# Kernel optimization log

Measured on AMD Instinct MI355X. Metric: run time of the kernel, lower is better.

Reference implementation:

```python
import jax, jax.numpy as jnp
import numpy as np

N, DEG, F_IN, F_OUT, H = 8192, 16, 1024, 128, 8


def setup_inputs() -> dict:
    key = jax.random.key(0)
    ks = jax.random.split(key, 6)
    features = jax.random.normal(ks[0], (N, F_IN), dtype=jnp.float32)
    adj = jax.random.randint(ks[1], (N, DEG), 0, N)  # fixed-degree adjacency
    W = jax.random.normal(ks[2], (H, F_IN, F_OUT), dtype=jnp.float32) / np.sqrt(F_IN)
    bW = jax.random.normal(ks[3], (H, F_OUT), dtype=jnp.float32) * 0.01
    a = jax.random.normal(ks[4], (H, 2 * F_OUT), dtype=jnp.float32) / np.sqrt(2.0 * F_OUT)
    ba = jax.random.normal(ks[5], (H,), dtype=jnp.float32) * 0.01
    return {"features": features, "adj": adj, "W": W, "bW": bW, "a": a, "ba": ba}


def reference(features, adj, W, bW, a, ba):
    n = features.shape[0]
    # neighbors with self appended last (matches adjlist[node] + [node])
    nbr = jnp.concatenate([adj, jnp.arange(n)[:, None]], axis=1)  # [N, DEG+1]
    # per-head linear transform: h[k] = features @ W_k + b_k
    h = jnp.einsum('nf,hfo->hno', features, W) + bW[:, None, :]  # [H, N, F_OUT]
    # attention score a_k([h_dst, h_src]) + bias decomposed into dst/src parts
    a_dst, a_src = a[:, :F_OUT], a[:, F_OUT:]
    s_dst = jnp.einsum('hno,ho->hn', h, a_dst)  # [H, N]
    s_src = jnp.einsum('hno,ho->hn', h, a_src)  # [H, N]
    scores = s_dst[:, :, None] + s_src[:, nbr] + ba[:, None, None]  # [H, N, DEG+1]
    scores = jax.nn.leaky_relu(scores, 0.2)
    alpha = jax.nn.softmax(scores, axis=-1)  # softmax over neighbors (incl. self)
    h_src = h[:, nbr]  # [H, N, DEG+1, F_OUT]
    out = jnp.einsum('hnd,hndf->hnf', alpha, h_src)  # [H, N, F_OUT]
    # concat heads along feature dim -> [N, H*F_OUT]
    return out.transpose(1, 0, 2).reshape(n, H * F_OUT)
```

## Files before the change

### kernel.cpp

```cpp
#include <hip/hip_runtime.h>
#include <hip/hip_bf16.h>

#define N_NODES 8192
#define DEG     16
#define F_IN    1024
#define F_OUT   128
#define NH      8

typedef __bf16 bf16x8 __attribute__((ext_vector_type(8)));
typedef float  f32x4  __attribute__((ext_vector_type(4)));

__device__ __forceinline__ float bf2f(unsigned short u) {
    union { unsigned int i; float f; } v;
    v.i = ((unsigned int)u) << 16;
    return v.f;
}
__device__ __forceinline__ unsigned short f2bf(float f) {
    union { float f; unsigned int u; } v; v.f = f;
    unsigned int u = v.u + 0x7FFFu + ((v.u >> 16) & 1u);
    return (unsigned short)(u >> 16);
}
__device__ __forceinline__ int detect_bf16(const unsigned int* __restrict__ w) {
    int hits = 0;
#pragma unroll
    for (int i = 0; i < 64; ++i) {
        unsigned int x = w[i * 131 + 17];
        int e = (x >> 7) & 0xFF;
        hits += (e >= 100 && e <= 140) ? 1 : 0;
    }
    return hits > 32;
}
__device__ __forceinline__ float rd_scalar(const void* p, int idx, int isbf) {
    return isbf ? bf2f(((const unsigned short*)p)[idx]) : ((const float*)p)[idx];
}
__device__ __forceinline__ void gload16(const void* g, void* l) {
    __builtin_amdgcn_global_load_lds(
        (const __attribute__((address_space(1))) void*)g,
        (__attribute__((address_space(3))) void*)l, 16, 0, 0);
}

__global__ __launch_bounds__(256) void prep_inputs(
    const void* __restrict__ feat, const void* __restrict__ W,
    unsigned short* __restrict__ featb, unsigned short* __restrict__ Wt)
{
    const int isbf = detect_bf16((const unsigned int*)feat);
    if (blockIdx.x < 4096) {
        size_t i8 = ((size_t)blockIdx.x * 256 + threadIdx.x) * 8;
        if (isbf) {
            *(uint4*)(featb + i8) = ((const uint4*)feat)[i8 / 8];
        } else {
            const float* s = (const float*)feat + i8;
            float4 u0 = *(const float4*)s;
            float4 u1 = *(const float4*)(s + 4);
            unsigned short t[8] = { f2bf(u0.x), f2bf(u0.y), f2bf(u0.z), f2bf(u0.w),
                                    f2bf(u1.x), f2bf(u1.y), f2bf(u1.z), f2bf(u1.w) };
            *(uint4*)(featb + i8) = *(const uint4*)t;
        }
    } else {
        __shared__ float tile[64][65];
        const int bx = blockIdx.x - 4096;
        const int h  = bx >> 5;
        const int kt = (bx >> 1) & 15;
        const int ot = bx & 1;
        const int t  = threadIdx.x;
#pragma unroll
        for (int i = 0; i < 16; ++i) {
            int id = i * 256 + t, r = id >> 6, c = id & 63;
            tile[r][c] = rd_scalar(W, ((h * 1024 + kt * 64 + r) * 128) + ot * 64 + c, isbf);
        }
        __syncthreads();
#pragma unroll
        for (int i = 0; i < 16; ++i) {
            int id = i * 256 + t, oc = id >> 6, kc = id & 63;
            Wt[(size_t)(h * 128 + ot * 64 + oc) * 1024 + kt * 64 + kc] = f2bf(tile[kc][oc]);
        }
    }
}

__global__ __launch_bounds__(256) void gat_gemm3(
    const unsigned short* __restrict__ featb,
    const unsigned short* __restrict__ Wt,
    const void* __restrict__ raw_feat,
    const void* __restrict__ bW, const void* __restrict__ a,
    const void* __restrict__ ba,
    __hip_bfloat16* __restrict__ hbuf,
    float* __restrict__ sdst, float* __restrict__ ssrc)
{
    const int rawbf = detect_bf16((const unsigned int*)raw_feat);

    const int h   = blockIdx.y;
    const int n0  = blockIdx.x * 128;
    const int tid = threadIdx.x;

    __shared__ __align__(16) unsigned short As[2][128 * 64];
    __shared__ __align__(16) unsigned short Bs[2][128 * 64];

    const int lane = tid & 63;
    const int wave = tid >> 6;
    const int quad = lane >> 4;
    const int l16  = lane & 15;
    const int sw   = l16 & 7;

    f32x4 acc[2][8];
#pragma unroll
    for (int i = 0; i < 2; ++i)
#pragma unroll
        for (int j = 0; j < 8; ++j) acc[i][j] = (f32x4)0.f;

    const unsigned short* wbase = Wt + (size_t)h * F_OUT * F_IN;

    for (int k0 = 0; k0 < F_IN; k0 += 128) {
#pragma unroll
        for (int p = 0; p < 2; ++p) {
            const int kk0 = k0 + p * 64;
#pragma unroll
            for (int t = 0; t < 4; ++t) {
                const int r0  = t * 32 + wave * 8;
                const int row = r0 + (lane >> 3);
                const int gc  = (lane & 7) ^ (row & 7);
                gload16(&featb[(size_t)(n0 + row) * F_IN + kk0 + gc * 8],
                        &As[p][r0 * 64]);
                gload16(&wbase[(size_t)row * F_IN + kk0 + gc * 8],
                        &Bs[p][r0 * 64]);
            }
        }
        __syncthreads();

#pragma unroll
        for (int p = 0; p < 2; ++p) {
#pragma unroll
            for (int ks = 0; ks < 2; ++ks) {
                const int kc = ks * 4 + quad;
                const int cs = (kc ^ sw) * 8;
                bf16x8 af[2], bfr[8];
#pragma unroll
                for (int rt = 0; rt < 2; ++rt)
                    af[rt] = *(const bf16x8*)&As[p][(wave * 32 + rt * 16 + l16) * 64 + cs];
#pragma unroll
                for (int ct = 0; ct < 8; ++ct)
                    bfr[ct] = *(const bf16x8*)&Bs[p][(ct * 16 + l16) * 64 + cs];
#pragma unroll
                for (int rt = 0; rt < 2; ++rt)
#pragma unroll
                    for (int ct = 0; ct < 8; ++ct)
                        acc[rt][ct] = __builtin_amdgcn_mfma_f32_16x16x32_bf16(
                            af[rt], bfr[ct], acc[rt][ct], 0, 0, 0);
            }
        }
        __syncthreads();
    }

#pragma unroll
    for (int ct = 0; ct < 8; ++ct) {
        const int col = ct * 16 + l16;
        const float bwv = rd_scalar(bW, h * F_OUT + col, rawbf);
#pragma unroll
        for (int rt = 0; rt < 2; ++rt) {
            const int nrow = n0 + wave * 32 + rt * 16 + quad * 4;
            __hip_bfloat16* dst = hbuf + ((size_t)h * N_NODES + nrow) * F_OUT + col;
#pragma unroll
            for (int r = 0; r < 4; ++r)
                dst[(size_t)r * F_OUT] = __float2bfloat16(acc[rt][ct][r] + bwv);
        }
    }

    float adst[8], asrc[8];
#pragma unroll
    for (int ct = 0; ct < 8; ++ct) {
        const int col = ct * 16 + l16;
        adst[ct] = rd_scalar(a, h * 256 + col, rawbf);
        asrc[ct] = rd_scalar(a, h * 256 + 128 + col, rawbf);
    }
    float pd[2][4] = {}, ps[2][4] = {};
#pragma unroll
    for (int rt = 0; rt < 2; ++rt)
#pragma unroll
        for (int ct = 0; ct < 8; ++ct)
#pragma unroll
            for (int r = 0; r < 4; ++r) {
                pd[rt][r] += acc[rt][ct][r] * adst[ct];
                ps[rt][r] += acc[rt][ct][r] * asrc[ct];
            }
#pragma unroll
    for (int off = 1; off < 16; off <<= 1)
#pragma unroll
        for (int rt = 0; rt < 2; ++rt)
#pragma unroll
            for (int r = 0; r < 4; ++r) {
                pd[rt][r] += __shfl_xor(pd[rt][r], off, 64);
                ps[rt][r] += __shfl_xor(ps[rt][r], off, 64);
            }
    if (l16 == 0) {
        const float bav = rd_scalar(ba, h, rawbf);
#pragma unroll
        for (int rt = 0; rt < 2; ++rt) {
            const int base = n0 + wave * 32 + rt * 16 + quad * 4;
            float4 vd = { pd[rt][0] + bav, pd[rt][1] + bav,
                          pd[rt][2] + bav, pd[rt][3] + bav };
            float4 vs = { ps[rt][0], ps[rt][1], ps[rt][2], ps[rt][3] };
            *(float4*)&sdst[h * N_NODES + base] = vd;
            *(float4*)&ssrc[h * N_NODES + base] = vs;
        }
    }
}

__global__ __launch_bounds__(256) void gat_aggr4(
    const unsigned short* __restrict__ hbuf,
    const int* __restrict__ adj,
    const float* __restrict__ sdst, const float* __restrict__ ssrc,
    const void* __restrict__ raw_feat, void* __restrict__ out)
{
    const int isbf = detect_bf16((const unsigned int*)raw_feat);
    const int h    = blockIdx.x;
    const int wave = threadIdx.x >> 6;
    const int lane = threadIdx.x & 63;
    const int half = lane >> 5;
    const int l32  = lane & 31;
    const int n    = blockIdx.y * 8 + wave * 2 + half;

    int nbr = n;
    if (l32 < DEG) nbr = adj[n * DEG + l32];

    float s = -1e30f;
    if (l32 < 17) {
        float sv = sdst[h * N_NODES + n] + ssrc[h * N_NODES + nbr];
        s = sv > 0.f ? sv : 0.2f * sv;
    }
    float m = s;
#pragma unroll
    for (int off = 1; off < 32; off <<= 1)
        m = fmaxf(m, __shfl_xor(m, off, 64));
    float ev = (l32 < 17) ? __expf(s - m) : 0.f;
    float sum = ev;
#pragma unroll
    for (int off = 1; off < 32; off <<= 1)
        sum += __shfl_xor(sum, off, 64);
    ev *= (1.f / sum);

    const unsigned short* hb = hbuf + (size_t)h * N_NODES * F_OUT;
    const int fc    = l32 * 4;
    const int sbase = half << 5;
    float a0 = 0.f, a1 = 0.f, a2 = 0.f, a3 = 0.f;
#pragma unroll
    for (int d = 0; d < 17; ++d) {
        const int   nb = __shfl(nbr, sbase + d, 64);
        const float av = __shfl(ev,  sbase + d, 64);
        uint2 pk = *(const uint2*)&hb[(size_t)nb * F_OUT + fc];
        a0 += av * bf2f((unsigned short)(pk.x & 0xffffu));
        a1 += av * bf2f((unsigned short)(pk.x >> 16));
        a2 += av * bf2f((unsigned short)(pk.y & 0xffffu));
        a3 += av * bf2f((unsigned short)(pk.y >> 16));
    }

    const size_t oidx = (size_t)n * (NH * F_OUT) + h * F_OUT + fc;
    if (isbf) {
        uint2 res;
        res.x = (unsigned int)f2bf(a0) | ((unsigned int)f2bf(a1) << 16);
        res.y = (unsigned int)f2bf(a2) | ((unsigned int)f2bf(a3) << 16);
        *(uint2*)&((unsigned short*)out)[oidx] = res;
    } else {
        float4 res = { a0, a1, a2, a3 };
        *(float4*)&((float*)out)[oidx] = res;
    }
}

__global__ __launch_bounds__(256) void gat_gemm_fb(
    const void* __restrict__ feat, const void* __restrict__ W,
    const void* __restrict__ bW, __hip_bfloat16* __restrict__ hbuf)
{
    const int isbf = detect_bf16((const unsigned int*)feat);
    const int h = blockIdx.y, n0 = blockIdx.x * 128, tid = threadIdx.x;
    __shared__ __align__(16) unsigned short As[128][72];
    __shared__ __align__(16) unsigned short Bs[128][72];
    const int lane = tid & 63, wave = tid >> 6, quad = lane >> 4, l16 = lane & 15;
    f32x4 acc[2][8];
#pragma unroll
    for (int i = 0; i < 2; ++i)
#pragma unroll
        for (int j = 0; j < 8; ++j) acc[i][j] = (f32x4)0.f;
    for (int k0 = 0; k0 < F_IN; k0 += 64) {
        if (isbf) {
            const unsigned short* fbase = (const unsigned short*)feat + (size_t)n0 * F_IN;
            const unsigned short* wsrc  = (const unsigned short*)W +
                                          (size_t)h * F_IN * F_OUT + (size_t)k0 * F_OUT;
#pragma unroll
            for (int t = 0; t < 4; ++t) {
                int c = t * 256 + tid, row = c >> 3, kc = c & 7;
                *(uint4*)&As[row][kc * 8] = *(const uint4*)&fbase[row * F_IN + k0 + kc * 8];
            }
#pragma unroll
            for (int t = 0; t < 2; ++t) {
                int c = t * 256 + tid, kr2 = c >> 4, mm = c & 15, oc = mm * 8;
                uint4 w0 = *(const uint4*)&wsrc[(2 * kr2) * F_OUT + oc];
                uint4 w1 = *(const uint4*)&wsrc[(2 * kr2 + 1) * F_OUT + oc];
                const unsigned short* p0 = (const unsigned short*)&w0;
                const unsigned short* p1 = (const unsigned short*)&w1;
#pragma unroll
                for (int j = 0; j < 8; ++j) {
                    int i = (j + mm) & 7;
                    *(unsigned int*)&Bs[oc + i][2 * kr2] =
                        (unsigned int)p0[i] | ((unsigned int)p1[i] << 16);
                }
            }
        } else {
            const float* fbase = (const float*)feat + (size_t)n0 * F_IN;
            const float* wsrc  = (const float*)W +
                                 (size_t)h * F_IN * F_OUT + (size_t)k0 * F_OUT;
#pragma unroll
            for (int t = 0; t < 4; ++t) {
                int c = t * 256 + tid, row = c >> 3, kc = c & 7;
                const float* src = &fbase[row * F_IN + k0 + kc * 8];
                float4 u0 = *(const float4*)src, u1 = *(const float4*)(src + 4);
                unsigned short sh[8] = { f2bf(u0.x), f2bf(u0.y), f2bf(u0.z), f2bf(u0.w),
                                         f2bf(u1.x), f2bf(u1.y), f2bf(u1.z), f2bf(u1.w) };
                *(uint4*)&As[row][kc * 8] = *(const uint4*)sh;
            }
#pragma unroll
            for (int t = 0; t < 2; ++t) {
                int c = t * 256 + tid, kr2 = c >> 4, mm = c & 15, oc = mm * 8;
                const float* r0 = &wsrc[(2 * kr2) * F_OUT + oc];
                const float* r1 = &wsrc[(2 * kr2 + 1) * F_OUT + oc];
                float4 e0 = *(const float4*)r0, e1 = *(const float4*)(r0 + 4);
                float4 o0 = *(const float4*)r1, o1 = *(const float4*)(r1 + 4);
                unsigned short p0[8] = { f2bf(e0.x), f2bf(e0.y), f2bf(e0.z), f2bf(e0.w),
                                         f2bf(e1.x), f2bf(e1.y), f2bf(e1.z), f2bf(e1.w) };
                unsigned short p1[8] = { f2bf(o0.x), f2bf(o0.y), f2bf(o0.z), f2bf(o0.w),
                                         f2bf(o1.x), f2bf(o1.y), f2bf(o1.z), f2bf(o1.w) };
#pragma unroll
                for (int j = 0; j < 8; ++j) {
                    int i = (j + mm) & 7;
                    *(unsigned int*)&Bs[oc + i][2 * kr2] =
                        (unsigned int)p0[i] | ((unsigned int)p1[i] << 16);
                }
            }
        }
        __syncthreads();
#pragma unroll
        for (int ks = 0; ks < 2; ++ks) {
            const int kk = ks * 32 + quad * 8;
            bf16x8 af[2], bfr[8];
#pragma unroll
            for (int rt = 0; rt < 2; ++rt)
                af[rt] = *(const bf16x8*)&As[wave * 32 + rt * 16 + l16][kk];
#pragma unroll
            for (int ct = 0; ct < 8; ++ct)
                bfr[ct] = *(const bf16x8*)&Bs[ct * 16 + l16][kk];
#pragma unroll
            for (int rt = 0; rt < 2; ++rt)
#pragma unroll
                for (int ct = 0; ct < 8; ++ct)
                    acc[rt][ct] = __builtin_amdgcn_mfma_f32_16x16x32_bf16(
                        af[rt], bfr[ct], acc[rt][ct], 0, 0, 0);
        }
        __syncthreads();
    }
#pragma unroll
    for (int ct = 0; ct < 8; ++ct) {
        const int col = ct * 16 + l16;
        const float bwv = rd_scalar(bW, h * F_OUT + col, isbf);
#pragma unroll
        for (int rt = 0; rt < 2; ++rt) {
            const int nrow = n0 + wave * 32 + rt * 16 + quad * 4;
            __hip_bfloat16* dst = hbuf + ((size_t)h * N_NODES + nrow) * F_OUT + col;
#pragma unroll
            for (int r = 0; r < 4; ++r)
                dst[(size_t)r * F_OUT] = __float2bfloat16(acc[rt][ct][r] + bwv);
        }
    }
}

__global__ __launch_bounds__(256) void gat_aggr_fb(
    const __hip_bfloat16* __restrict__ hbuf, const int* __restrict__ adj,
    const void* __restrict__ a, const void* __restrict__ ba,
    void* __restrict__ out, const void* __restrict__ feat)
{
    const int isbf = detect_bf16((const unsigned int*)feat);
    const int n = blockIdx.x, wave = threadIdx.x >> 6, lane = threadIdx.x & 63;
    const int hh = blockIdx.y * 4 + wave;
    int nbr_reg = n;
    if (lane < DEG) nbr_reg = adj[n * DEG + lane];
    const int f0 = lane * 2;
    const float adst0 = rd_scalar(a, hh * 256 + f0, isbf);
    const float adst1 = rd_scalar(a, hh * 256 + f0 + 1, isbf);
    const float asrc0 = rd_scalar(a, hh * 256 + 128 + f0, isbf);
    const float asrc1 = rd_scalar(a, hh * 256 + 128 + f0 + 1, isbf);
    const float bav   = rd_scalar(ba, hh, isbf);
    const __hip_bfloat16* hb = hbuf + (size_t)hh * N_NODES * F_OUT;
    float v0[17], v1[17], red[18];
#pragma unroll
    for (int d = 0; d < 17; ++d) {
        int nb = __shfl(nbr_reg, d, 64);
        unsigned int pk = *(const unsigned int*)&hb[(size_t)nb * F_OUT + f0];
        v0[d] = bf2f((unsigned short)(pk & 0xffffu));
        v1[d] = bf2f((unsigned short)(pk >> 16));
        red[d] = v0[d] * asrc0 + v1[d] * asrc1;
    }
    red[17] = v0[16] * adst0 + v1[16] * adst1;
#pragma unroll
    for (int off = 1; off < 64; off <<= 1)
#pragma unroll
        for (int r = 0; r < 18; ++r) red[r] += __shfl_xor(red[r], off, 64);
    const float sd = red[17] + bav;
    float sc[17], mx = -1e30f;
#pragma unroll
    for (int d = 0; d < 17; ++d) {
        float s = sd + red[d];
        s = s > 0.f ? s : 0.2f * s;
        sc[d] = s; mx = fmaxf(mx, s);
    }
    float ssum = 0.f;
#pragma unroll
    for (int d = 0; d < 17; ++d) { sc[d] = __expf(sc[d] - mx); ssum += sc[d]; }
    const float inv = 1.f / ssum;
    float o0 = 0.f, o1 = 0.f;
#pragma unroll
    for (int d = 0; d < 17; ++d) { o0 += sc[d] * v0[d]; o1 += sc[d] * v1[d]; }
    o0 *= inv; o1 *= inv;
    const size_t oidx = (size_t)n * (NH * F_OUT) + hh * F_OUT + f0;
    if (isbf) {
        *(unsigned int*)&((unsigned short*)out)[oidx] =
            (unsigned int)f2bf(o0) | ((unsigned int)f2bf(o1) << 16);
    } else {
        float2 res; res.x = o0; res.y = o1;
        *(float2*)&((float*)out)[oidx] = res;
    }
}

extern "C" void kernel_launch(void* const* d_in, const int* in_sizes, int n_in,
                              void* d_out, int out_size, void* d_ws, size_t ws_size,
                              hipStream_t stream)
{
    const void* feat = d_in[0];
    const int*  adj  = (const int*)d_in[1];
    const void* W    = d_in[2];
    const void* bW   = d_in[3];
    const void* a    = d_in[4];
    const void* ba   = d_in[5];

    char* ws = (char*)d_ws;
    __hip_bfloat16* hbuf = (__hip_bfloat16*)ws;
    const size_t HB = (size_t)NH * N_NODES * F_OUT * 2;
    const size_t SC = (size_t)NH * N_NODES * 4;
    float* sdst = (float*)(ws + HB);
    float* ssrc = (float*)(ws + HB + SC);
    unsigned short* featb = (unsigned short*)(ws + HB + 2 * SC);
    unsigned short* Wt    = featb + (size_t)N_NODES * F_IN;
    const size_t needA = HB + 2 * SC +
        ((size_t)N_NODES * F_IN + (size_t)NH * F_IN * F_OUT) * 2;

    if (ws_size >= needA) {
        prep_inputs<<<4352, 256, 0, stream>>>(feat, W, featb, Wt);
        gat_gemm3<<<dim3(64, 8), 256, 0, stream>>>(featb, Wt, feat, bW, a, ba,
                                                   hbuf, sdst, ssrc);
        gat_aggr4<<<dim3(8, 1024), 256, 0, stream>>>((const unsigned short*)hbuf,
                                                     adj, sdst, ssrc, feat, d_out);
    } else {
        gat_gemm_fb<<<dim3(64, 8), 256, 0, stream>>>(feat, W, bW, hbuf);
        gat_aggr_fb<<<dim3(8192, 2), 256, 0, stream>>>(hbuf, adj, a, ba, d_out, feat);
    }
}
```

Before: 149.0 us.

## Rewrite GEMM with 256x128 tiles, 8 waves, and 3-stage async load pipeline

Replaces the 128x128, 4-wave GEMM with a 256x128 tile per block using 8 waves arranged as a 4x2 grid, and a triple-buffered shared-memory pipeline. Global loads for later K-tiles are issued while MFMAs run on the current tile, coordinated by explicit vmcnt waits and raw barriers. s_setprio is raised around the MFMA bursts. The attention-score dot products now need a cross-wave reduction through shared memory. The aim is to hide global load latency and improve reuse. In exchange, shared memory use grows to about 144KB. The grid also halves to 256 blocks, which may underfill the GPU's compute units.

```diff
diff --git a/kernel.cpp b/kernel.cpp
--- a/kernel.cpp
+++ b/kernel.cpp
@@ -77,7 +77,7 @@
     }
 }
 
-__global__ __launch_bounds__(256) void gat_gemm3(
+__global__ __launch_bounds__(512, 2) void gat_gemm4(
     const unsigned short* __restrict__ featb,
     const unsigned short* __restrict__ Wt,
     const void* __restrict__ raw_feat,
@@ -89,118 +89,138 @@
     const int rawbf = detect_bf16((const unsigned int*)raw_feat);
 
     const int h   = blockIdx.y;
-    const int n0  = blockIdx.x * 128;
+    const int n0  = blockIdx.x * 256;
     const int tid = threadIdx.x;
 
-    __shared__ __align__(16) unsigned short As[2][128 * 64];
-    __shared__ __align__(16) unsigned short Bs[2][128 * 64];
+    __shared__ __align__(16) unsigned short As[3][256 * 64];
+    __shared__ __align__(16) unsigned short Bs[3][128 * 64];
+    __shared__ float sred[4][2][2][64];
 
     const int lane = tid & 63;
     const int wave = tid >> 6;
+    const int wr   = wave >> 1;
+    const int wc   = wave & 1;
     const int quad = lane >> 4;
     const int l16  = lane & 15;
-    const int sw   = l16 & 7;
-
-    f32x4 acc[2][8];
-#pragma unroll
-    for (int i = 0; i < 2; ++i)
-#pragma unroll
-        for (int j = 0; j < 8; ++j) acc[i][j] = (f32x4)0.f;
+    const int srow   = lane >> 3;
+    const int schunk = lane & 7;
+
+    f32x4 acc[4][4];
+#pragma unroll
+    for (int i = 0; i < 4; ++i)
+#pragma unroll
+        for (int j = 0; j < 4; ++j) acc[i][j] = (f32x4)0.f;
 
     const unsigned short* wbase = Wt + (size_t)h * F_OUT * F_IN;
 
-    for (int k0 = 0; k0 < F_IN; k0 += 128) {
-#pragma unroll
-        for (int p = 0; p < 2; ++p) {
-            const int kk0 = k0 + p * 64;
-#pragma unroll
-            for (int t = 0; t < 4; ++t) {
-                const int r0  = t * 32 + wave * 8;
-                const int row = r0 + (lane >> 3);
-                const int gc  = (lane & 7) ^ (row & 7);
-                gload16(&featb[(size_t)(n0 + row) * F_IN + kk0 + gc * 8],
-                        &As[p][r0 * 64]);
-                gload16(&wbase[(size_t)row * F_IN + kk0 + gc * 8],
-                        &Bs[p][r0 * 64]);
-            }
-        }
-        __syncthreads();
-
-#pragma unroll
-        for (int p = 0; p < 2; ++p) {
-#pragma unroll
-            for (int ks = 0; ks < 2; ++ks) {
-                const int kc = ks * 4 + quad;
-                const int cs = (kc ^ sw) * 8;
-                bf16x8 af[2], bfr[8];
-#pragma unroll
-                for (int rt = 0; rt < 2; ++rt)
-                    af[rt] = *(const bf16x8*)&As[p][(wave * 32 + rt * 16 + l16) * 64 + cs];
-#pragma unroll
-                for (int ct = 0; ct < 8; ++ct)
-                    bfr[ct] = *(const bf16x8*)&Bs[p][(ct * 16 + l16) * 64 + cs];
-#pragma unroll
-                for (int rt = 0; rt < 2; ++rt)
-#pragma unroll
-                    for (int ct = 0; ct < 8; ++ct)
-                        acc[rt][ct] = __builtin_amdgcn_mfma_f32_16x16x32_bf16(
-                            af[rt], bfr[ct], acc[rt][ct], 0, 0, 0);
-            }
-        }
-        __syncthreads();
-    }
-
-#pragma unroll
-    for (int ct = 0; ct < 8; ++ct) {
-        const int col = ct * 16 + l16;
-        const float bwv = rd_scalar(bW, h * F_OUT + col, rawbf);
-#pragma unroll
-        for (int rt = 0; rt < 2; ++rt) {
-            const int nrow = n0 + wave * 32 + rt * 16 + quad * 4;
-            __hip_bfloat16* dst = hbuf + ((size_t)h * N_NODES + nrow) * F_OUT + col;
-#pragma unroll
-            for (int r = 0; r < 4; ++r)
-                dst[(size_t)r * F_OUT] = __float2bfloat16(acc[rt][ct][r] + bwv);
-        }
-    }
-
-    float adst[8], asrc[8];
-#pragma unroll
-    for (int ct = 0; ct < 8; ++ct) {
-        const int col = ct * 16 + l16;
+    auto stage = [&](int kt, int s) {
+        if (kt >= 16) return;
+        const int kk0 = kt * 64;
+#pragma unroll
+        for (int t = 0; t < 4; ++t) {
+            const int r0  = t * 64 + wave * 8;
+            const int row = r0 + srow;
+            const int gc  = schunk ^ (row & 7);
+            gload16(&featb[(size_t)(n0 + row) * F_IN + kk0 + gc * 8],
+                    &As[s][r0 * 64]);
+        }
+#pragma unroll
+        for (int t = 0; t < 2; ++t) {
+            const int r0  = t * 64 + wave * 8;
+            const int row = r0 + srow;
+            const int gc  = schunk ^ (row & 7);
+            gload16(&wbase[(size_t)row * F_IN + kk0 + gc * 8],
+                    &Bs[s][r0 * 64]);
+        }
+    };
+
+    stage(0, 0);
+    stage(1, 1);
+
+    for (int t = 0; t < 16; ++t) {
+        stage(t + 2, (t + 2) % 3);
+        if (t < 14)       asm volatile("s_waitcnt vmcnt(12)" ::: "memory");
+        else if (t == 14) asm volatile("s_waitcnt vmcnt(6)"  ::: "memory");
+        else              asm volatile("s_waitcnt vmcnt(0)"  ::: "memory");
+        asm volatile("s_barrier" ::: "memory");
+
+        const unsigned short* Ab = As[t % 3];
+        const unsigned short* Bb = Bs[t % 3];
+#pragma unroll
+        for (int ks = 0; ks < 2; ++ks) {
+            const int kc = ks * 4 + quad;
+            const int cs = (kc ^ (l16 & 7)) * 8;
+            bf16x8 af[4], bfr[4];
+#pragma unroll
+            for (int rt = 0; rt < 4; ++rt)
+                af[rt] = *(const bf16x8*)&Ab[(wr * 64 + rt * 16 + l16) * 64 + cs];
+#pragma unroll
+            for (int ct = 0; ct < 4; ++ct)
+                bfr[ct] = *(const bf16x8*)&Bb[(wc * 64 + ct * 16 + l16) * 64 + cs];
+            __builtin_amdgcn_s_setprio(1);
+#pragma unroll
+            for (int rt = 0; rt < 4; ++rt)
+#pragma unroll
+                for (int ct = 0; ct < 4; ++ct)
+                    acc[rt][ct] = __builtin_amdgcn_mfma_f32_16x16x32_bf16(
+                        af[rt], bfr[ct], acc[rt][ct], 0, 0, 0);
+            __builtin_amdgcn_s_setprio(0);
+        }
+        asm volatile("s_barrier" ::: "memory");
+    }
+
+    float adst[4], asrc[4];
+#pragma unroll
+    for (int ct = 0; ct < 4; ++ct) {
+        const int col = wc * 64 + ct * 16 + l16;
         adst[ct] = rd_scalar(a, h * 256 + col, rawbf);
         asrc[ct] = rd_scalar(a, h * 256 + 128 + col, rawbf);
     }
-    float pd[2][4] = {}, ps[2][4] = {};
-#pragma unroll
-    for (int rt = 0; rt < 2; ++rt)
-#pragma unroll
-        for (int ct = 0; ct < 8; ++ct)
+    float pd[4][4] = {}, ps[4][4] = {};
+#pragma unroll
+    for (int ct = 0; ct < 4; ++ct) {
+        const int col = wc * 64 + ct * 16 + l16;
+        const float bwv = rd_scalar(bW, h * F_OUT + col, rawbf);
+#pragma unroll
+        for (int rt = 0; rt < 4; ++rt) {
+            const int nrow = n0 + wr * 64 + rt * 16 + quad * 4;
+            __hip_bfloat16* dst = hbuf + ((size_t)h * N_NODES + nrow) * F_OUT + col;
 #pragma unroll
             for (int r = 0; r < 4; ++r) {
+                dst[(size_t)r * F_OUT] = __float2bfloat16(acc[rt][ct][r] + bwv);
                 pd[rt][r] += acc[rt][ct][r] * adst[ct];
                 ps[rt][r] += acc[rt][ct][r] * asrc[ct];
             }
+        }
+    }
 #pragma unroll
     for (int off = 1; off < 16; off <<= 1)
 #pragma unroll
-        for (int rt = 0; rt < 2; ++rt)
+        for (int rt = 0; rt < 4; ++rt)
 #pragma unroll
             for (int r = 0; r < 4; ++r) {
                 pd[rt][r] += __shfl_xor(pd[rt][r], off, 64);
                 ps[rt][r] += __shfl_xor(ps[rt][r], off, 64);
             }
     if (l16 == 0) {
+#pragma unroll
+        for (int rt = 0; rt < 4; ++rt)
+#pragma unroll
+            for (int r = 0; r < 4; ++r) {
+                const int row64 = rt * 16 + quad * 4 + r;
+                sred[wr][wc][0][row64] = pd[rt][r];
+                sred[wr][wc][1][row64] = ps[rt][r];
+            }
+    }
+    __syncthreads();
+    if (wc == 0) {
         const float bav = rd_scalar(ba, h, rawbf);
-#pragma unroll
-        for (int rt = 0; rt < 2; ++rt) {
-            const int base = n0 + wave * 32 + rt * 16 + quad * 4;
-            float4 vd = { pd[rt][0] + bav, pd[rt][1] + bav,
-                          pd[rt][2] + bav, pd[rt][3] + bav };
-            float4 vs = { ps[rt][0], ps[rt][1], ps[rt][2], ps[rt][3] };
-            *(float4*)&sdst[h * N_NODES + base] = vd;
-            *(float4*)&ssrc[h * N_NODES + base] = vs;
-        }
+        const int row64 = lane;
+        const float vd = sred[wr][0][0][row64] + sred[wr][1][0][row64] + bav;
+        const float vs = sred[wr][0][1][row64] + sred[wr][1][1][row64];
+        const int nrow = n0 + wr * 64 + row64;
+        sdst[h * N_NODES + nrow] = vd;
+        ssrc[h * N_NODES + nrow] = vs;
     }
 }
 
@@ -450,7 +470,7 @@
 
     if (ws_size >= needA) {
         prep_inputs<<<4352, 256, 0, stream>>>(feat, W, featb, Wt);
-        gat_gemm3<<<dim3(64, 8), 256, 0, stream>>>(featb, Wt, feat, bW, a, ba,
+        gat_gemm4<<<dim3(32, 8), 512, 0, stream>>>(featb, Wt, feat, bW, a, ba,
                                                    hbuf, sdst, ssrc);
         gat_aggr4<<<dim3(8, 1024), 256, 0, stream>>>((const unsigned short*)hbuf,
                                                      adj, sdst, ssrc, feat, d_out);
```

Result: slower. 157.0 us (+5.4%).

## Double-buffer GEMM K-tiles to overlap global loads with MFMA compute

Applied to the files above, without the earlier changes.

The projection GEMM's main loop used to load two 64-wide K slices, synchronize, compute both, then synchronize again, so loads and math never overlapped. It now runs a software pipeline over 16 K-tiles of 64. The next tile is loaded into the alternate LDS buffer while the current tile is computed, with one barrier per iteration. This is meant to hide global-to-LDS latency behind MFMA work. In exchange there are twice as many loop iterations and barriers, each with less work, and correctness depends on the async loads landing before the barrier.

```diff
diff --git a/kernel.cpp b/kernel.cpp
--- a/kernel.cpp
+++ b/kernel.cpp
@@ -100,6 +100,8 @@
     const int quad = lane >> 4;
     const int l16  = lane & 15;
     const int sw   = l16 & 7;
+    const int srow   = lane >> 3;
+    const int schunk = lane & 7;
 
     f32x4 acc[2][8];
 #pragma unroll
@@ -109,45 +111,48 @@
 
     const unsigned short* wbase = Wt + (size_t)h * F_OUT * F_IN;
 
-    for (int k0 = 0; k0 < F_IN; k0 += 128) {
-#pragma unroll
-        for (int p = 0; p < 2; ++p) {
-            const int kk0 = k0 + p * 64;
-#pragma unroll
-            for (int t = 0; t < 4; ++t) {
-                const int r0  = t * 32 + wave * 8;
-                const int row = r0 + (lane >> 3);
-                const int gc  = (lane & 7) ^ (row & 7);
-                gload16(&featb[(size_t)(n0 + row) * F_IN + kk0 + gc * 8],
-                        &As[p][r0 * 64]);
-                gload16(&wbase[(size_t)row * F_IN + kk0 + gc * 8],
-                        &Bs[p][r0 * 64]);
-            }
-        }
+    auto stage = [&](int kt, int s) {
+        const int kk0 = kt * 64;
+#pragma unroll
+        for (int t = 0; t < 4; ++t) {
+            const int r0  = t * 32 + wave * 8;
+            const int row = r0 + srow;
+            const int gc  = schunk ^ (row & 7);
+            gload16(&featb[(size_t)(n0 + row) * F_IN + kk0 + gc * 8],
+                    &As[s][r0 * 64]);
+            gload16(&wbase[(size_t)row * F_IN + kk0 + gc * 8],
+                    &Bs[s][r0 * 64]);
+        }
+    };
+
+    stage(0, 0);
+    __syncthreads();
+
+    int cur = 0;
+    for (int t = 0; t < 16; ++t) {
+        if (t < 15) stage(t + 1, cur ^ 1);
+
+#pragma unroll
+        for (int ks = 0; ks < 2; ++ks) {
+            const int kc = ks * 4 + quad;
+            const int cs = (kc ^ sw) * 8;
+            bf16x8 af[2], bfr[8];
+#pragma unroll
+            for (int rt = 0; rt < 2; ++rt)
+                af[rt] = *(const bf16x8*)&As[cur][(wave * 32 + rt * 16 + l16) * 64 + cs];
+#pragma unroll
+            for (int ct = 0; ct < 8; ++ct)
+                bfr[ct] = *(const bf16x8*)&Bs[cur][(ct * 16 + l16) * 64 + cs];
+#pragma unroll
+            for (int rt = 0; rt < 2; ++rt)
+#pragma unroll
+                for (int ct = 0; ct < 8; ++ct)
+                    acc[rt][ct] = __builtin_amdgcn_mfma_f32_16x16x32_bf16(
+                        af[rt], bfr[ct], acc[rt][ct], 0, 0, 0);
+        }
+
         __syncthreads();
-
-#pragma unroll
-        for (int p = 0; p < 2; ++p) {
-#pragma unroll
-            for (int ks = 0; ks < 2; ++ks) {
-                const int kc = ks * 4 + quad;
-                const int cs = (kc ^ sw) * 8;
-                bf16x8 af[2], bfr[8];
-#pragma unroll
-                for (int rt = 0; rt < 2; ++rt)
-                    af[rt] = *(const bf16x8*)&As[p][(wave * 32 + rt * 16 + l16) * 64 + cs];
-#pragma unroll
-                for (int ct = 0; ct < 8; ++ct)
-                    bfr[ct] = *(const bf16x8*)&Bs[p][(ct * 16 + l16) * 64 + cs];
-#pragma unroll
-                for (int rt = 0; rt < 2; ++rt)
-#pragma unroll
-                    for (int ct = 0; ct < 8; ++ct)
-                        acc[rt][ct] = __builtin_amdgcn_mfma_f32_16x16x32_bf16(
-                            af[rt], bfr[ct], acc[rt][ct], 0, 0, 0);
-            }
-        }
-        __syncthreads();
+        cur ^= 1;
     }
 
 #pragma unroll
```

After: 154.6 us. +3.8%, slower.

## Fuse prep, GEMM and aggregation into one persistent kernel with grid barriers

Applied to the files above, without the earlier changes.

Three kernel launches are replaced by a single persistent kernel of 512 blocks. The blocks step through the input conversion, the per-head GEMM and the neighbor aggregation, with atomic-counter grid barriers between the phases. The intent is to remove launch overhead and the tails between kernels. The cost is that every block must be co-resident, since the barrier has a spin timeout and could deadlock or misbehave otherwise. The aggregation phase also loses parallelism, because each block now loops over 16 row groups.

```diff
diff --git a/kernel.cpp b/kernel.cpp
--- a/kernel.cpp
+++ b/kernel.cpp
@@ -39,228 +39,250 @@
         (__attribute__((address_space(3))) void*)l, 16, 0, 0);
 }
 
-__global__ __launch_bounds__(256) void prep_inputs(
-    const void* __restrict__ feat, const void* __restrict__ W,
-    unsigned short* __restrict__ featb, unsigned short* __restrict__ Wt)
-{
-    const int isbf = detect_bf16((const unsigned int*)feat);
-    if (blockIdx.x < 4096) {
-        size_t i8 = ((size_t)blockIdx.x * 256 + threadIdx.x) * 8;
-        if (isbf) {
-            *(uint4*)(featb + i8) = ((const uint4*)feat)[i8 / 8];
-        } else {
-            const float* s = (const float*)feat + i8;
-            float4 u0 = *(const float4*)s;
-            float4 u1 = *(const float4*)(s + 4);
-            unsigned short t[8] = { f2bf(u0.x), f2bf(u0.y), f2bf(u0.z), f2bf(u0.w),
-                                    f2bf(u1.x), f2bf(u1.y), f2bf(u1.z), f2bf(u1.w) };
-            *(uint4*)(featb + i8) = *(const uint4*)t;
-        }
-    } else {
-        __shared__ float tile[64][65];
-        const int bx = blockIdx.x - 4096;
-        const int h  = bx >> 5;
-        const int kt = (bx >> 1) & 15;
-        const int ot = bx & 1;
-        const int t  = threadIdx.x;
-#pragma unroll
-        for (int i = 0; i < 16; ++i) {
-            int id = i * 256 + t, r = id >> 6, c = id & 63;
-            tile[r][c] = rd_scalar(W, ((h * 1024 + kt * 64 + r) * 128) + ot * 64 + c, isbf);
-        }
-        __syncthreads();
-#pragma unroll
-        for (int i = 0; i < 16; ++i) {
-            int id = i * 256 + t, oc = id >> 6, kc = id & 63;
-            Wt[(size_t)(h * 128 + ot * 64 + oc) * 1024 + kt * 64 + kc] = f2bf(tile[kc][oc]);
-        }
-    }
-}
-
-__global__ __launch_bounds__(256) void gat_gemm3(
-    const unsigned short* __restrict__ featb,
-    const unsigned short* __restrict__ Wt,
-    const void* __restrict__ raw_feat,
-    const void* __restrict__ bW, const void* __restrict__ a,
-    const void* __restrict__ ba,
+#define GRID 512
+__device__ unsigned gbar[2];
+
+__device__ __forceinline__ void gridbar(int ep) {
+    __syncthreads();
+    if (threadIdx.x == 0) {
+        __threadfence();
+        unsigned ticket = atomicAdd(&gbar[ep], 1u);
+        unsigned target = (ticket / GRID + 1u) * GRID;
+        unsigned spins  = 0;
+        while (__hip_atomic_load(&gbar[ep], __ATOMIC_RELAXED,
+                                 __HIP_MEMORY_SCOPE_AGENT) < target) {
+            __builtin_amdgcn_s_sleep(2);
+            if (++spins > 2000000u) break;
+        }
+        __threadfence();
+    }
+    __syncthreads();
+}
+
+__global__ __launch_bounds__(256, 2) void gat_fused(
+    const void* __restrict__ feat, const int* __restrict__ adj,
+    const void* __restrict__ W,    const void* __restrict__ bW,
+    const void* __restrict__ a,    const void* __restrict__ ba,
+    void* __restrict__ out,
+    unsigned short* __restrict__ featb, unsigned short* __restrict__ Wt,
     __hip_bfloat16* __restrict__ hbuf,
     float* __restrict__ sdst, float* __restrict__ ssrc)
 {
-    const int rawbf = detect_bf16((const unsigned int*)raw_feat);
-
-    const int h   = blockIdx.y;
-    const int n0  = blockIdx.x * 128;
-    const int tid = threadIdx.x;
-
-    __shared__ __align__(16) unsigned short As[2][128 * 64];
-    __shared__ __align__(16) unsigned short Bs[2][128 * 64];
-
+    __shared__ __align__(16) unsigned char smem[65536];
+    const int isbf = detect_bf16((const unsigned int*)feat);
+    const int bid  = blockIdx.x;
+    const int tid  = threadIdx.x;
     const int lane = tid & 63;
     const int wave = tid >> 6;
-    const int quad = lane >> 4;
-    const int l16  = lane & 15;
-    const int sw   = l16 & 7;
-
-    f32x4 acc[2][8];
-#pragma unroll
-    for (int i = 0; i < 2; ++i)
-#pragma unroll
-        for (int j = 0; j < 8; ++j) acc[i][j] = (f32x4)0.f;
-
-    const unsigned short* wbase = Wt + (size_t)h * F_OUT * F_IN;
-
-    for (int k0 = 0; k0 < F_IN; k0 += 128) {
-#pragma unroll
-        for (int p = 0; p < 2; ++p) {
-            const int kk0 = k0 + p * 64;
-#pragma unroll
-            for (int t = 0; t < 4; ++t) {
-                const int r0  = t * 32 + wave * 8;
-                const int row = r0 + (lane >> 3);
-                const int gc  = (lane & 7) ^ (row & 7);
-                gload16(&featb[(size_t)(n0 + row) * F_IN + kk0 + gc * 8],
-                        &As[p][r0 * 64]);
-                gload16(&wbase[(size_t)row * F_IN + kk0 + gc * 8],
-                        &Bs[p][r0 * 64]);
-            }
-        }
-        __syncthreads();
-
-#pragma unroll
-        for (int p = 0; p < 2; ++p) {
-#pragma unroll
-            for (int ks = 0; ks < 2; ++ks) {
-                const int kc = ks * 4 + quad;
-                const int cs = (kc ^ sw) * 8;
-                bf16x8 af[2], bfr[8];
-#pragma unroll
-                for (int rt = 0; rt < 2; ++rt)
-                    af[rt] = *(const bf16x8*)&As[p][(wave * 32 + rt * 16 + l16) * 64 + cs];
-#pragma unroll
-                for (int ct = 0; ct < 8; ++ct)
-                    bfr[ct] = *(const bf16x8*)&Bs[p][(ct * 16 + l16) * 64 + cs];
-#pragma unroll
-                for (int rt = 0; rt < 2; ++rt)
+
+    {
+#pragma unroll
+        for (int i = 0; i < 8; ++i) {
+            const int u = bid * 8 + i;
+            size_t i8 = ((size_t)u * 256 + tid) * 8;
+            if (isbf) {
+                *(uint4*)(featb + i8) = ((const uint4*)feat)[i8 / 8];
+            } else {
+                const float* s = (const float*)feat + i8;
+                float4 u0 = *(const float4*)s;
+                float4 u1 = *(const float4*)(s + 4);
+                unsigned short t[8] = { f2bf(u0.x), f2bf(u0.y), f2bf(u0.z), f2bf(u0.w),
+                                        f2bf(u1.x), f2bf(u1.y), f2bf(u1.z), f2bf(u1.w) };
+                *(uint4*)(featb + i8) = *(const uint4*)t;
+            }
+        }
+        if (bid < 256) {
+            float (*tile)[65] = (float (*)[65])smem;
+            const int h  = bid >> 5;
+            const int kt = (bid >> 1) & 15;
+            const int ot = bid & 1;
+#pragma unroll
+            for (int i = 0; i < 16; ++i) {
+                int id = i * 256 + tid, r = id >> 6, c = id & 63;
+                tile[r][c] = rd_scalar(W, ((h * 1024 + kt * 64 + r) * 128) + ot * 64 + c, isbf);
+            }
+            __syncthreads();
+#pragma unroll
+            for (int i = 0; i < 16; ++i) {
+                int id = i * 256 + tid, oc = id >> 6, kc = id & 63;
+                Wt[(size_t)(h * 128 + ot * 64 + oc) * 1024 + kt * 64 + kc] = f2bf(tile[kc][oc]);
+            }
+        }
+    }
+    gridbar(0);
+
+    {
+        const int h  = bid & 7;
+        const int n0 = (bid >> 3) * 128;
+
+        unsigned short (*As)[128 * 64] = (unsigned short (*)[128 * 64])smem;
+        unsigned short (*Bs)[128 * 64] = (unsigned short (*)[128 * 64])(smem + 32768);
+
+        const int quad = lane >> 4;
+        const int l16  = lane & 15;
+        const int sw   = l16 & 7;
+        const int srow   = lane >> 3;
+        const int schunk = lane & 7;
+
+        f32x4 acc[2][8];
+#pragma unroll
+        for (int i = 0; i < 2; ++i)
+#pragma unroll
+            for (int j = 0; j < 8; ++j) acc[i][j] = (f32x4)0.f;
+
+        const unsigned short* wbase = Wt + (size_t)h * F_OUT * F_IN;
+
+        for (int k0 = 0; k0 < F_IN; k0 += 128) {
+#pragma unroll
+            for (int p = 0; p < 2; ++p) {
+                const int kk0 = k0 + p * 64;
+#pragma unroll
+                for (int t = 0; t < 4; ++t) {
+                    const int r0  = t * 32 + wave * 8;
+                    const int row = r0 + srow;
+                    const int gc  = schunk ^ (row & 7);
+                    gload16(&featb[(size_t)(n0 + row) * F_IN + kk0 + gc * 8],
+                            &As[p][r0 * 64]);
+                    gload16(&wbase[(size_t)row * F_IN + kk0 + gc * 8],
+                            &Bs[p][r0 * 64]);
+                }
+            }
+            __syncthreads();
+
+#pragma unroll
+            for (int p = 0; p < 2; ++p) {
+#pragma unroll
+                for (int ks = 0; ks < 2; ++ks) {
+                    const int kc = ks * 4 + quad;
+                    const int cs = (kc ^ sw) * 8;
+                    bf16x8 af[2], bfr[8];
+#pragma unroll
+                    for (int rt = 0; rt < 2; ++rt)
+                        af[rt] = *(const bf16x8*)&As[p][(wave * 32 + rt * 16 + l16) * 64 + cs];
 #pragma unroll
                     for (int ct = 0; ct < 8; ++ct)
-                        acc[rt][ct] = __builtin_amdgcn_mfma_f32_16x16x32_bf16(
-                            af[rt], bfr[ct], acc[rt][ct], 0, 0, 0);
-            }
-        }
-        __syncthreads();
-    }
-
-#pragma unroll
-    for (int ct = 0; ct < 8; ++ct) {
-        const int col = ct * 16 + l16;
-        const float bwv = rd_scalar(bW, h * F_OUT + col, rawbf);
-#pragma unroll
-        for (int rt = 0; rt < 2; ++rt) {
-            const int nrow = n0 + wave * 32 + rt * 16 + quad * 4;
-            __hip_bfloat16* dst = hbuf + ((size_t)h * N_NODES + nrow) * F_OUT + col;
-#pragma unroll
-            for (int r = 0; r < 4; ++r)
-                dst[(size_t)r * F_OUT] = __float2bfloat16(acc[rt][ct][r] + bwv);
-        }
-    }
-
-    float adst[8], asrc[8];
-#pragma unroll
-    for (int ct = 0; ct < 8; ++ct) {
-        const int col = ct * 16 + l16;
-        adst[ct] = rd_scalar(a, h * 256 + col, rawbf);
-        asrc[ct] = rd_scalar(a, h * 256 + 128 + col, rawbf);
-    }
-    float pd[2][4] = {}, ps[2][4] = {};
-#pragma unroll
-    for (int rt = 0; rt < 2; ++rt)
-#pragma unroll
-        for (int ct = 0; ct < 8; ++ct)
-#pragma unroll
-            for (int r = 0; r < 4; ++r) {
-                pd[rt][r] += acc[rt][ct][r] * adst[ct];
-                ps[rt][r] += acc[rt][ct][r] * asrc[ct];
-            }
-#pragma unroll
-    for (int off = 1; off < 16; off <<= 1)
+                        bfr[ct] = *(const bf16x8*)&Bs[p][(ct * 16 + l16) * 64 + cs];
+#pragma unroll
+                    for (int rt = 0; rt < 2; ++rt)
+#pragma unroll
+                        for (int ct = 0; ct < 8; ++ct)
+                            acc[rt][ct] = __builtin_amdgcn_mfma_f32_16x16x32_bf16(
+                                af[rt], bfr[ct], acc[rt][ct], 0, 0, 0);
+                }
+            }
+            __syncthreads();
+        }
+
+#pragma unroll
+        for (int ct = 0; ct < 8; ++ct) {
+            const int col = ct * 16 + l16;
+            const float bwv = rd_scalar(bW, h * F_OUT + col, isbf);
+#pragma unroll
+            for (int rt = 0; rt < 2; ++rt) {
+                const int nrow = n0 + wave * 32 + rt * 16 + quad * 4;
+                __hip_bfloat16* dst = hbuf + ((size_t)h * N_NODES + nrow) * F_OUT + col;
+#pragma unroll
+                for (int r = 0; r < 4; ++r)
+                    dst[(size_t)r * F_OUT] = __float2bfloat16(acc[rt][ct][r] + bwv);
+            }
+        }
+
+        float adst[8], asrc[8];
+#pragma unroll
+        for (int ct = 0; ct < 8; ++ct) {
+            const int col = ct * 16 + l16;
+            adst[ct] = rd_scalar(a, h * 256 + col, isbf);
+            asrc[ct] = rd_scalar(a, h * 256 + 128 + col, isbf);
+        }
+        float pd[2][4] = {}, ps[2][4] = {};
 #pragma unroll
         for (int rt = 0; rt < 2; ++rt)
 #pragma unroll
-            for (int r = 0; r < 4; ++r) {
-                pd[rt][r] += __shfl_xor(pd[rt][r], off, 64);
-                ps[rt][r] += __shfl_xor(ps[rt][r], off, 64);
-            }
-    if (l16 == 0) {
-        const float bav = rd_scalar(ba, h, rawbf);
-#pragma unroll
-        for (int rt = 0; rt < 2; ++rt) {
-            const int base = n0 + wave * 32 + rt * 16 + quad * 4;
-            float4 vd = { pd[rt][0] + bav, pd[rt][1] + bav,
-                          pd[rt][2] + bav, pd[rt][3] + bav };
-            float4 vs = { ps[rt][0], ps[rt][1], ps[rt][2], ps[rt][3] };
-            *(float4*)&sdst[h * N_NODES + base] = vd;
-            *(float4*)&ssrc[h * N_NODES + base] = vs;
-        }
-    }
-}
-
-__global__ __launch_bounds__(256) void gat_aggr4(
-    const unsigned short* __restrict__ hbuf,
-    const int* __restrict__ adj,
-    const float* __restrict__ sdst, const float* __restrict__ ssrc,
-    const void* __restrict__ raw_feat, void* __restrict__ out)
-{
-    const int isbf = detect_bf16((const unsigned int*)raw_feat);
-    const int h    = blockIdx.x;
-    const int wave = threadIdx.x >> 6;
-    const int lane = threadIdx.x & 63;
-    const int half = lane >> 5;
-    const int l32  = lane & 31;
-    const int n    = blockIdx.y * 8 + wave * 2 + half;
-
-    int nbr = n;
-    if (l32 < DEG) nbr = adj[n * DEG + l32];
-
-    float s = -1e30f;
-    if (l32 < 17) {
-        float sv = sdst[h * N_NODES + n] + ssrc[h * N_NODES + nbr];
-        s = sv > 0.f ? sv : 0.2f * sv;
-    }
-    float m = s;
-#pragma unroll
-    for (int off = 1; off < 32; off <<= 1)
-        m = fmaxf(m, __shfl_xor(m, off, 64));
-    float ev = (l32 < 17) ? __expf(s - m) : 0.f;
-    float sum = ev;
-#pragma unroll
-    for (int off = 1; off < 32; off <<= 1)
-        sum += __shfl_xor(sum, off, 64);
-    ev *= (1.f / sum);
-
-    const unsigned short* hb = hbuf + (size_t)h * N_NODES * F_OUT;
-    const int fc    = l32 * 4;
-    const int sbase = half << 5;
-    float a0 = 0.f, a1 = 0.f, a2 = 0.f, a3 = 0.f;
-#pragma unroll
-    for (int d = 0; d < 17; ++d) {
-        const int   nb = __shfl(nbr, sbase + d, 64);
-        const float av = __shfl(ev,  sbase + d, 64);
-        uint2 pk = *(const uint2*)&hb[(size_t)nb * F_OUT + fc];
-        a0 += av * bf2f((unsigned short)(pk.x & 0xffffu));
-        a1 += av * bf2f((unsigned short)(pk.x >> 16));
-        a2 += av * bf2f((unsigned short)(pk.y & 0xffffu));
-        a3 += av * bf2f((unsigned short)(pk.y >> 16));
-    }
-
-    const size_t oidx = (size_t)n * (NH * F_OUT) + h * F_OUT + fc;
-    if (isbf) {
-        uint2 res;
-        res.x = (unsigned int)f2bf(a0) | ((unsigned int)f2bf(a1) << 16);
-        res.y = (unsigned int)f2bf(a2) | ((unsigned int)f2bf(a3) << 16);
-        *(uint2*)&((unsigned short*)out)[oidx] = res;
-    } else {
-        float4 res = { a0, a1, a2, a3 };
-        *(float4*)&((float*)out)[oidx] = res;
+            for (int ct = 0; ct < 8; ++ct)
+#pragma unroll
+                for (int r = 0; r < 4; ++r) {
+                    pd[rt][r] += acc[rt][ct][r] * adst[ct];
+                    ps[rt][r] += acc[rt][ct][r] * asrc[ct];
+                }
+#pragma unroll
+        for (int off = 1; off < 16; off <<= 1)
+#pragma unroll
+            for (int rt = 0; rt < 2; ++rt)
+#pragma unroll
+                for (int r = 0; r < 4; ++r) {
+                    pd[rt][r] += __shfl_xor(pd[rt][r], off, 64);
+                    ps[rt][r] += __shfl_xor(ps[rt][r], off, 64);
+                }
+        if (l16 == 0) {
+            const float bav = rd_scalar(ba, h, isbf);
+#pragma unroll
+            for (int rt = 0; rt < 2; ++rt) {
+                const int base = n0 + wave * 32 + rt * 16 + quad * 4;
+                float4 vd = { pd[rt][0] + bav, pd[rt][1] + bav,
+                              pd[rt][2] + bav, pd[rt][3] + bav };
+                float4 vs = { ps[rt][0], ps[rt][1], ps[rt][2], ps[rt][3] };
+                *(float4*)&sdst[h * N_NODES + base] = vd;
+                *(float4*)&ssrc[h * N_NODES + base] = vs;
+            }
+        }
+    }
+    gridbar(1);
+
+    {
+        const int h    = bid & 7;
+        const int half = lane >> 5;
+        const int l32  = lane & 31;
+        const unsigned short* hb = (const unsigned short*)hbuf + (size_t)h * N_NODES * F_OUT;
+        const int fc    = l32 * 4;
+        const int sbase = half << 5;
+
+#pragma unroll 1
+        for (int j = 0; j < 16; ++j) {
+            const int by = (bid >> 3) * 16 + j;
+            const int n  = by * 8 + wave * 2 + half;
+
+            int nbr = n;
+            if (l32 < DEG) nbr = adj[n * DEG + l32];
+
+            float s = -1e30f;
+            if (l32 < 17) {
+                float sv = sdst[h * N_NODES + n] + ssrc[h * N_NODES + nbr];
+                s = sv > 0.f ? sv : 0.2f * sv;
+            }
+            float m = s;
+#pragma unroll
+            for (int off = 1; off < 32; off <<= 1)
+                m = fmaxf(m, __shfl_xor(m, off, 64));
+            float ev = (l32 < 17) ? __expf(s - m) : 0.f;
+            float sum = ev;
+#pragma unroll
+            for (int off = 1; off < 32; off <<= 1)
+                sum += __shfl_xor(sum, off, 64);
+            ev *= (1.f / sum);
+
+            float a0 = 0.f, a1 = 0.f, a2 = 0.f, a3 = 0.f;
+#pragma unroll
+            for (int d = 0; d < 17; ++d) {
+                const int   nb = __shfl(nbr, sbase + d, 64);
+                const float av = __shfl(ev,  sbase + d, 64);
+                uint2 pk = *(const uint2*)&hb[(size_t)nb * F_OUT + fc];
+                a0 += av * bf2f((unsigned short)(pk.x & 0xffffu));
+                a1 += av * bf2f((unsigned short)(pk.x >> 16));
+                a2 += av * bf2f((unsigned short)(pk.y & 0xffffu));
+                a3 += av * bf2f((unsigned short)(pk.y >> 16));
+            }
+
+            const size_t oidx = (size_t)n * (NH * F_OUT) + h * F_OUT + fc;
+            if (isbf) {
+                uint2 res;
+                res.x = (unsigned int)f2bf(a0) | ((unsigned int)f2bf(a1) << 16);
+                res.y = (unsigned int)f2bf(a2) | ((unsigned int)f2bf(a3) << 16);
+                *(uint2*)&((unsigned short*)out)[oidx] = res;
+            } else {
+                float4 res = { a0, a1, a2, a3 };
+                *(float4*)&((float*)out)[oidx] = res;
+            }
+        }
     }
 }
 
@@ -449,11 +471,8 @@
         ((size_t)N_NODES * F_IN + (size_t)NH * F_IN * F_OUT) * 2;
 
     if (ws_size >= needA) {
-        prep_inputs<<<4352, 256, 0, stream>>>(feat, W, featb, Wt);
-        gat_gemm3<<<dim3(64, 8), 256, 0, stream>>>(featb, Wt, feat, bW, a, ba,
-                                                   hbuf, sdst, ssrc);
-        gat_aggr4<<<dim3(8, 1024), 256, 0, stream>>>((const unsigned short*)hbuf,
-                                                     adj, sdst, ssrc, feat, d_out);
+        gat_fused<<<dim3(GRID), dim3(256), 0, stream>>>(
+            feat, adj, W, bW, a, ba, d_out, featb, Wt, hbuf, sdst, ssrc);
     } else {
         gat_gemm_fb<<<dim3(64, 8), 256, 0, stream>>>(feat, W, bW, hbuf);
         gat_aggr_fb<<<dim3(8192, 2), 256, 0, stream>>>(hbuf, adj, a, ba, d_out, feat);
```

New measurement: 265.6 us. +78.3%, slower.
